# Kernel optimization log

Hardware: AMD Instinct MI355X
Metric: run time of the kernel (lower is better)

## Reference

```python
import jax, jax.numpy as jnp
import numpy as np

B, T_IN, F, H = 256, 168, 128, 512
T_OUT = 48


def setup_inputs() -> dict:
    key = jax.random.key(0)
    ks = jax.random.split(key, 8)
    s = 1.0 / np.sqrt(H)
    return {
        "x": jax.random.normal(ks[0], (B, T_IN, F), dtype=jnp.float32),
        "enc_Wih": jax.random.normal(ks[1], (4 * H, F), dtype=jnp.float32) * s,
        "enc_Whh": jax.random.normal(ks[2], (4 * H, H), dtype=jnp.float32) * s,
        "enc_b": jax.random.normal(ks[3], (4 * H,), dtype=jnp.float32) * s,
        "dec_Wih": jax.random.normal(ks[4], (4 * H, F), dtype=jnp.float32) * s,
        "dec_Whh": jax.random.normal(ks[5], (4 * H, H), dtype=jnp.float32) * s,
        "dec_b": jax.random.normal(ks[6], (4 * H,), dtype=jnp.float32) * s,
        "W_lin": jax.random.normal(ks[7], (F, H), dtype=jnp.float32) * s,
        "t_out": T_OUT,
    }


def _lstm_cell(h, c, xt, Wih, Whh, b):
    # torch gate order: i, f, g, o
    gates = xt @ Wih.T + h @ Whh.T + b  # [B, 4H]
    i, f, g, o = jnp.split(gates, 4, axis=-1)
    c_new = jax.nn.sigmoid(f) * c + jax.nn.sigmoid(i) * jnp.tanh(g)
    h_new = jax.nn.sigmoid(o) * jnp.tanh(c_new)
    return h_new, c_new


def reference(x, enc_Wih, enc_Whh, enc_b, dec_Wih, dec_Whh, dec_b, W_lin, t_out):
    bsz = x.shape[0]
    hidden = enc_Whh.shape[1]
    h0 = jnp.zeros((bsz, hidden), x.dtype)
    c0 = jnp.zeros((bsz, hidden), x.dtype)

    # ---- encoder: scan over T_in ----
    def enc_step(carry, xt):
        h, c = carry
        h, c = _lstm_cell(h, c, xt, enc_Wih, enc_Whh, enc_b)
        return (h, c), None

    (hn, cn), _ = jax.lax.scan(enc_step, (h0, c0), jnp.swapaxes(x, 0, 1))

    # ---- decoder: recursive feeding, scan over T_out ----
    dec_in0 = x[:, -1, :]  # [B, F]

    def dec_step(carry, _):
        h, c, inp = carry
        h, c = _lstm_cell(h, c, inp, dec_Wih, dec_Whh, dec_b)
        out = h @ W_lin.T  # [B, F]
        return (h, c, out), out

    _, outs = jax.lax.scan(dec_step, (hn, cn, dec_in0), None, length=t_out)
    return jnp.swapaxes(outs, 0, 1)  # [B, T_out, F]
```

## Files before the change

kernel.cpp:

```cpp
#include <hip/hip_runtime.h>
#include <hip/hip_bf16.h>

typedef __bf16 bf16_t;
typedef __bf16 bf16x8 __attribute__((ext_vector_type(8)));
typedef __bf16 bf16x4 __attribute__((ext_vector_type(4)));
typedef float  f32x4  __attribute__((ext_vector_type(4)));

#define HID 512
#define BATCH 256
#define TIN 168
#define TOUT 48
#define FEAT 128
#define NSTEPS (TIN + TOUT)
#define NGRP 8
#define NJT 32
#define GRPB 32

__device__ __forceinline__ float sigmoidf_(float x) {
    x = fminf(fmaxf(x, -30.f), 30.f);
    return 1.f / (1.f + __expf(-x));
}
__device__ __forceinline__ float tanhf_(float x) {
    x = fminf(fmaxf(x, -15.f), 15.f);
    float e = __expf(2.f * x);
    return (e - 1.f) / (e + 1.f);
}

__device__ __forceinline__ bf16x8 ld_h8(const bf16_t* p) {
    union { unsigned long long q[2]; bf16x8 v; } u;
    u.q[0] = __hip_atomic_load((const unsigned long long*)p,     __ATOMIC_RELAXED,
                               __HIP_MEMORY_SCOPE_SYSTEM);
    u.q[1] = __hip_atomic_load((const unsigned long long*)p + 1, __ATOMIC_RELAXED,
                               __HIP_MEMORY_SCOPE_SYSTEM);
    return u.v;
}
__device__ __forceinline__ void st_h(bf16_t* p, float v) {
    bf16_t b = (bf16_t)v;
    unsigned short u;
    __builtin_memcpy(&u, &b, 2);
    __hip_atomic_store((unsigned short*)p, u, __ATOMIC_RELAXED, __HIP_MEMORY_SCOPE_SYSTEM);
}

__global__ __launch_bounds__(256)
void cast_x_kernel(const float* __restrict__ x, bf16_t* __restrict__ Xbf) {
    int q = blockIdx.x * 256 + threadIdx.x;
    if (q >= BATCH * TIN * (FEAT / 4)) return;
    int f4  = q & 31;
    int rem = q >> 5;
    int t = rem % TIN;
    int b = rem / TIN;
    float4 v = *(const float4*)&x[((size_t)b * TIN + t) * FEAT + f4 * 4];
    bf16x4 o = { (bf16_t)v.x, (bf16_t)v.y, (bf16_t)v.z, (bf16_t)v.w };
    *(bf16x4*)&Xbf[((size_t)t * BATCH + b) * FEAT + f4 * 4] = o;
}

__global__ __launch_bounds__(256)
void cast_wcat_kernel(const float* __restrict__ Wih, const float* __restrict__ Whh,
                      bf16_t* __restrict__ Wcat) {
    int q = blockIdx.x * 256 + threadIdx.x;
    int k4 = q % 160;
    int r  = q / 160;
    if (r >= 2048) return;
    int k = k4 * 4;
    float4 v;
    if (k < FEAT) v = *(const float4*)&Wih[(size_t)r * FEAT + k];
    else          v = *(const float4*)&Whh[(size_t)r * HID + (k - FEAT)];
    bf16x4 o = { (bf16_t)v.x, (bf16_t)v.y, (bf16_t)v.z, (bf16_t)v.w };
    *(bf16x4*)&Wcat[(size_t)r * 640 + k] = o;
}

__global__ __launch_bounds__(256)
void cast_wlin_kernel(const float* __restrict__ W, bf16_t* __restrict__ Wb) {
    int q = blockIdx.x * 256 + threadIdx.x;
    if (q >= FEAT * HID / 4) return;
    float4 v = *(const float4*)&W[q * 4];
    bf16x4 o = { (bf16_t)v.x, (bf16_t)v.y, (bf16_t)v.z, (bf16_t)v.w };
    *(bf16x4*)&Wb[q * 4] = o;
}

__global__ __launch_bounds__(256)
void build_wcomb_kernel(const float* __restrict__ dWih, const float* __restrict__ dWhh,
                        const float* __restrict__ Wlin, bf16_t* __restrict__ Wcomb) {
    __shared__ float As[64][128];
    __shared__ float Bs[128][64];
    int r0 = blockIdx.x * 64, c0 = blockIdx.y * 64;
    int tid = threadIdx.x;
    for (int i = tid; i < 64 * 32; i += 256) {
        int rr = i >> 5, cc = (i & 31) << 2;
        *(float4*)&As[rr][cc] = *(const float4*)&dWih[(size_t)(r0 + rr) * 128 + cc];
    }
    for (int i = tid; i < 128 * 16; i += 256) {
        int kk = i >> 4, cc = (i & 15) << 2;
        *(float4*)&Bs[kk][cc] = *(const float4*)&Wlin[(size_t)kk * HID + c0 + cc];
    }
    __syncthreads();
    int tx = tid & 15, ty = tid >> 4;
    float acc[4][4] = {};
    for (int k = 0; k < 128; ++k) {
        float a[4], b[4];
        #pragma unroll
        for (int i = 0; i < 4; ++i) a[i] = As[ty * 4 + i][k];
        #pragma unroll
        for (int j = 0; j < 4; ++j) b[j] = Bs[k][tx * 4 + j];
        #pragma unroll
        for (int i = 0; i < 4; ++i)
            #pragma unroll
            for (int j = 0; j < 4; ++j) acc[i][j] += a[i] * b[j];
    }
    for (int i = 0; i < 4; ++i) {
        int r = r0 + ty * 4 + i;
        for (int j = 0; j < 4; ++j) {
            int cc = c0 + tx * 4 + j;
            Wcomb[(size_t)r * HID + cc] = (bf16_t)(acc[i][j] + dWhh[(size_t)r * HID + cc]);
        }
    }
}


__device__ __forceinline__ void cell_finish(
    f32x4 (&acc)[4], float (&cacc)[4], float (*Ex)[GRPB][18],
    int gp, int bh, int l4, int l15, int b0, int jcol,
    bf16_t* __restrict__ hnext)
{
    if (gp == 1) {
        #pragma unroll
        for (int q = 0; q < 4; ++q)
            #pragma unroll
            for (int r = 0; r < 4; ++r)
                Ex[q][bh * 16 + l4 * 4 + r][l15] = acc[q][r];
    }
    __syncthreads();
    if (gp == 0) {
        #pragma unroll
        for (int q = 0; q < 4; ++q)
            #pragma unroll
            for (int r = 0; r < 4; ++r)
                acc[q][r] += Ex[q][bh * 16 + l4 * 4 + r][l15];
        #pragma unroll
        for (int r = 0; r < 4; ++r) {
            float cn = sigmoidf_(acc[1][r]) * cacc[r] + sigmoidf_(acc[0][r]) * tanhf_(acc[2][r]);
            cacc[r] = cn;
            float hv = sigmoidf_(acc[3][r]) * tanhf_(cn);
            int row = b0 + l4 * 4 + r;
            st_h(hnext + (size_t)row * HID + jcol, hv);
        }
        asm volatile("s_waitcnt vmcnt(0)" ::: "memory");
    }
    __syncthreads();
}

__device__ __forceinline__ void group_wait(const unsigned int* flags, int g, int tid,
                                           unsigned int epoch) {
    if (tid < NJT) {
        while (__hip_atomic_load(&flags[g * NJT + tid], __ATOMIC_RELAXED,
                                 __HIP_MEMORY_SCOPE_SYSTEM) < epoch)
            __builtin_amdgcn_s_sleep(1);
    }
    __syncthreads();
}

__device__ __forceinline__ void group_arrive(unsigned int* flags, int g, int jt, int tid,
                                             unsigned int epoch) {
    if (tid == 0)
        __hip_atomic_store(&flags[g * NJT + jt], epoch, __ATOMIC_RELAXED,
                           __HIP_MEMORY_SCOPE_SYSTEM);
}

__global__ __launch_bounds__(256, 1)
void lstm_persist(const bf16_t* __restrict__ Xbf,
                  const bf16_t* __restrict__ Wenc, const float* __restrict__ enc_b,
                  const bf16_t* __restrict__ Wdec1, const bf16_t* __restrict__ Wcomb,
                  const float* __restrict__ dec_b,
                  bf16_t* __restrict__ hbufA, bf16_t* __restrict__ hbufB,
                  bf16_t* __restrict__ Hdec, unsigned int* __restrict__ flags)
{
    __shared__ float Ex[4][GRPB][18];
    const int bid = blockIdx.x;
    const int g   = bid & (NGRP - 1);
    const int jt  = bid >> 3;
    const int j0  = jt * 16;
    const int tid = threadIdx.x;
    const int wave = tid >> 6, lane = tid & 63;
    const int l15 = lane & 15, l4 = lane >> 4;
    const int bh = wave & 1, gp = wave >> 1;
    const int b0 = g * GRPB + bh * 16;
    const int arow = b0 + l15;
    const int jcol = j0 + l15;

    float biasE[4], biasD[4];
    #pragma unroll
    for (int q = 0; q < 4; ++q) {
        biasE[q] = enc_b[q * HID + jcol];
        biasD[q] = dec_b[q * HID + jcol];
    }
    float cacc[4] = {0.f, 0.f, 0.f, 0.f};

    bf16x8 Breg[40];
    const int kc0 = gp * 320;

    #pragma unroll
    for (int q = 0; q < 4; ++q)
        #pragma unroll
        for (int i = 0; i < 10; ++i)
            Breg[q * 10 + i] = *(const bf16x8*)(
                Wenc + (size_t)(q * HID + jcol) * 640 + kc0 + i * 32 + l4 * 8);
    #pragma unroll
    for (int n = 0; n < 40; ++n) asm volatile("" : "+v"(Breg[n]));

    for (int t = 0; t < TIN; ++t) {
        if (t > 0) group_wait(flags, g, tid, (unsigned)t);
        const bf16_t* hb = (t & 1) ? hbufB : hbufA;
        bf16_t* hn       = (t & 1) ? hbufA : hbufB;
        f32x4 acc[4];
        #pragma unroll
        for (int q = 0; q < 4; ++q) {
            float bv = (gp == 0) ? biasE[q] : 0.f;
            acc[q] = (f32x4){bv, bv, bv, bv};
        }
        const bf16_t* xb  = Xbf + ((size_t)t * BATCH + arow) * FEAT + l4 * 8;
        const bf16_t* hbp = hb + (size_t)arow * HID + l4 * 8;
        #pragma unroll
        for (int i = 0; i < 10; ++i) {
            int kc = kc0 + i * 32;
            bf16x8 a;
            if (kc < FEAT) a = *(const bf16x8*)(xb + kc);
            else           a = ld_h8(hbp + (kc - FEAT));
            #pragma unroll
            for (int q = 0; q < 4; ++q)
                acc[q] = __builtin_amdgcn_mfma_f32_16x16x32_bf16(a, Breg[q * 10 + i], acc[q], 0, 0, 0);
        }
        cell_finish(acc, cacc, Ex, gp, bh, l4, l15, b0, jcol, hn);
        group_arrive(flags, g, jt, tid, (unsigned)(t + 1));
    }

    #pragma unroll
    for (int q = 0; q < 4; ++q)
        #pragma unroll
        for (int i = 0; i < 10; ++i)
            Breg[q * 10 + i] = *(const bf16x8*)(
                Wdec1 + (size_t)(q * HID + jcol) * 640 + kc0 + i * 32 + l4 * 8);
    #pragma unroll
    for (int n = 0; n < 40; ++n) asm volatile("" : "+v"(Breg[n]));

    {
        const int t = TIN;
        group_wait(flags, g, tid, (unsigned)t);
        f32x4 acc[4];
        #pragma unroll
        for (int q = 0; q < 4; ++q) {
            float bv = (gp == 0) ? biasD[q] : 0.f;
            acc[q] = (f32x4){bv, bv, bv, bv};
        }
        const bf16_t* xb  = Xbf + ((size_t)(TIN - 1) * BATCH + arow) * FEAT + l4 * 8;
        const bf16_t* hbp = hbufA + (size_t)arow * HID + l4 * 8;
        #pragma unroll
        for (int i = 0; i < 10; ++i) {
            int kc = kc0 + i * 32;
            bf16x8 a;
            if (kc < FEAT) a = *(const bf16x8*)(xb + kc);
            else           a = ld_h8(hbp + (kc - FEAT));
            #pragma unroll
            for (int q = 0; q < 4; ++q)
                acc[q] = __builtin_amdgcn_mfma_f32_16x16x32_bf16(a, Breg[q * 10 + i], acc[q], 0, 0, 0);
        }
        cell_finish(acc, cacc, Ex, gp, bh, l4, l15, b0, jcol, Hdec);
        group_arrive(flags, g, jt, tid, (unsigned)(t + 1));
    }

    const int kd0 = gp * 256;
    #pragma unroll
    for (int q = 0; q < 4; ++q)
        #pragma unroll
        for (int i = 0; i < 8; ++i)
            Breg[q * 8 + i] = *(const bf16x8*)(
                Wcomb + (size_t)(q * HID + jcol) * HID + kd0 + i * 32 + l4 * 8);
    #pragma unroll
    for (int n = 0; n < 32; ++n) asm volatile("" : "+v"(Breg[n]));

    for (int t = TIN + 1; t < NSTEPS; ++t) {
        group_wait(flags, g, tid, (unsigned)t);
        const bf16_t* hprev = Hdec + (size_t)(t - 1 - TIN) * BATCH * HID
                                   + (size_t)arow * HID + l4 * 8;
        f32x4 acc[4];
        #pragma unroll
        for (int q = 0; q < 4; ++q) {
            float bv = (gp == 0) ? biasD[q] : 0.f;
            acc[q] = (f32x4){bv, bv, bv, bv};
        }
        #pragma unroll
        for (int i = 0; i < 8; ++i) {
            bf16x8 a = ld_h8(hprev + kd0 + i * 32);
            #pragma unroll
            for (int q = 0; q < 4; ++q)
                acc[q] = __builtin_amdgcn_mfma_f32_16x16x32_bf16(a, Breg[q * 8 + i], acc[q], 0, 0, 0);
        }
        cell_finish(acc, cacc, Ex, gp, bh, l4, l15, b0, jcol,
                    Hdec + (size_t)(t - TIN) * BATCH * HID);
        group_arrive(flags, g, jt, tid, (unsigned)(t + 1));
    }
}

__global__ __launch_bounds__(128)
void final_proj_kernel(const bf16_t* __restrict__ Hdec, const bf16_t* __restrict__ Wlin,
                       float* __restrict__ out) {
    int tid = threadIdx.x;
    int wv = tid >> 6, lane = tid & 63;
    int l15 = lane & 15, l4 = lane >> 4;
    int row0 = blockIdx.x * 32 + wv * 16;
    const bf16_t* arow = Hdec + (size_t)(row0 + l15) * HID;
    f32x4 acc[8];
    #pragma unroll
    for (int n = 0; n < 8; ++n) acc[n] = (f32x4){0.f, 0.f, 0.f, 0.f};
    #pragma unroll 4
    for (int kc = 0; kc < HID; kc += 32) {
        bf16x8 af = *(const bf16x8*)(arow + kc + l4 * 8);
        #pragma unroll
        for (int n = 0; n < 8; ++n) {
            bf16x8 bfr = *(const bf16x8*)(Wlin + (size_t)(n * 16 + l15) * HID + kc + l4 * 8);
            acc[n] = __builtin_amdgcn_mfma_f32_16x16x32_bf16(af, bfr, acc[n], 0, 0, 0);
        }
    }
    #pragma unroll
    for (int n = 0; n < 8; ++n) {
        int f = n * 16 + l15;
        #pragma unroll
        for (int r = 0; r < 4; ++r) {
            int row = row0 + l4 * 4 + r;
            int t = row >> 8;
            int b = row & 255;
            out[(size_t)b * (TOUT * FEAT) + (size_t)t * FEAT + f] = acc[n][r];
        }
    }
}

extern "C" void kernel_launch(void* const* d_in, const int* in_sizes, int n_in,
                              void* d_out, int out_size, void* d_ws, size_t ws_size,
                              hipStream_t stream) {
    const float* x       = (const float*)d_in[0];
    const float* enc_Wih = (const float*)d_in[1];
    const float* enc_Whh = (const float*)d_in[2];
    const float* enc_b   = (const float*)d_in[3];
    const float* dec_Wih = (const float*)d_in[4];
    const float* dec_Whh = (const float*)d_in[5];
    const float* dec_b   = (const float*)d_in[6];
    const float* W_lin   = (const float*)d_in[7];
    float* out = (float*)d_out;

    char* p = (char*)d_ws;
    auto alloc = [&](size_t bytes) -> void* {
        void* r = (void*)p;
        p += (bytes + 255) & ~(size_t)255;
        return r;
    };
    bf16_t* Xbf    = (bf16_t*)alloc((size_t)TIN * BATCH * FEAT * 2);
    bf16_t* Wenc   = (bf16_t*)alloc((size_t)2048 * 640 * 2);
    bf16_t* Wdec1  = (bf16_t*)alloc((size_t)2048 * 640 * 2);
    bf16_t* Wcomb  = (bf16_t*)alloc((size_t)2048 * HID * 2);
    bf16_t* Wlinb  = (bf16_t*)alloc((size_t)FEAT * HID * 2);
    bf16_t* hbufA  = (bf16_t*)alloc((size_t)BATCH * HID * 2);
    bf16_t* hbufB  = (bf16_t*)alloc((size_t)BATCH * HID * 2);
    bf16_t* Hdec   = (bf16_t*)alloc((size_t)TOUT * BATCH * HID * 2);
    unsigned int* flags = (unsigned int*)alloc((size_t)NGRP * NJT * 4);

    (void)hipMemsetAsync(hbufA, 0, (size_t)BATCH * HID * 2, stream);
    (void)hipMemsetAsync(flags, 0, (size_t)NGRP * NJT * 4, stream);

    cast_x_kernel<<<(BATCH * TIN * (FEAT / 4) + 255) / 256, 256, 0, stream>>>(x, Xbf);
    cast_wcat_kernel<<<(2048 * 160 + 255) / 256, 256, 0, stream>>>(enc_Wih, enc_Whh, Wenc);
    cast_wcat_kernel<<<(2048 * 160 + 255) / 256, 256, 0, stream>>>(dec_Wih, dec_Whh, Wdec1);
    cast_wlin_kernel<<<(FEAT * HID / 4 + 255) / 256, 256, 0, stream>>>(W_lin, Wlinb);
    build_wcomb_kernel<<<dim3(2048 / 64, HID / 64), 256, 0, stream>>>(dec_Wih, dec_Whh, W_lin, Wcomb);

    lstm_persist<<<NGRP * NJT, 256, 0, stream>>>(Xbf, Wenc, enc_b, Wdec1, Wcomb, dec_b,
                                                 hbufA, hbufB, Hdec, flags);

    final_proj_kernel<<<(TOUT * BATCH) / 32, 128, 0, stream>>>(Hdec, Wlinb, out);
}
```

Measured before the change: 1.054 ms.

## Use agent-scope atomics when a group's blocks share one XCC, and vectorize h stores

At kernel start each block records its XCC id, and each batch group checks whether all 32 of its blocks landed on the same XCC. If they did, the recurrence runs with agent-scope atomic loads, stores and flags, which can stay in the shared L2 instead of going to system-coherent memory. Otherwise it falls back to system scope. Separately, h outputs are staged through LDS and written as 16-byte vector stores instead of scattered 2-byte atomics. The fast path relies on the block-to-XCC dispatch placement, and the XCC check spin-waits across all blocks, which assumes every block is co-resident.

```diff
diff --git a/kernel.cpp b/kernel.cpp
--- a/kernel.cpp
+++ b/kernel.cpp
@@ -5,6 +5,7 @@
 typedef __bf16 bf16x8 __attribute__((ext_vector_type(8)));
 typedef __bf16 bf16x4 __attribute__((ext_vector_type(4)));
 typedef float  f32x4  __attribute__((ext_vector_type(4)));
+typedef unsigned long long u64;
 
 #define HID 512
 #define BATCH 256
@@ -26,19 +27,19 @@
     return (e - 1.f) / (e + 1.f);
 }
 
+template <int SCOPE>
 __device__ __forceinline__ bf16x8 ld_h8(const bf16_t* p) {
-    union { unsigned long long q[2]; bf16x8 v; } u;
-    u.q[0] = __hip_atomic_load((const unsigned long long*)p,     __ATOMIC_RELAXED,
-                               __HIP_MEMORY_SCOPE_SYSTEM);
-    u.q[1] = __hip_atomic_load((const unsigned long long*)p + 1, __ATOMIC_RELAXED,
-                               __HIP_MEMORY_SCOPE_SYSTEM);
+    union { u64 q[2]; bf16x8 v; } u;
+    u.q[0] = __hip_atomic_load((const u64*)p,     __ATOMIC_RELAXED, SCOPE);
+    u.q[1] = __hip_atomic_load((const u64*)p + 1, __ATOMIC_RELAXED, SCOPE);
     return u.v;
 }
-__device__ __forceinline__ void st_h(bf16_t* p, float v) {
-    bf16_t b = (bf16_t)v;
-    unsigned short u;
-    __builtin_memcpy(&u, &b, 2);
-    __hip_atomic_store((unsigned short*)p, u, __ATOMIC_RELAXED, __HIP_MEMORY_SCOPE_SYSTEM);
+template <int SCOPE>
+__device__ __forceinline__ void st_h16(bf16_t* p, bf16x8 v) {
+    union { bf16x8 v; u64 q[2]; } u;
+    u.v = v;
+    __hip_atomic_store((u64*)p,     u.q[0], __ATOMIC_RELAXED, SCOPE);
+    __hip_atomic_store((u64*)p + 1, u.q[1], __ATOMIC_RELAXED, SCOPE);
 }
 
 __global__ __launch_bounds__(256)
@@ -117,9 +118,10 @@
 }
 
 
+template <int SCOPE>
 __device__ __forceinline__ void cell_finish(
-    f32x4 (&acc)[4], float (&cacc)[4], float (*Ex)[GRPB][18],
-    int gp, int bh, int l4, int l15, int b0, int jcol,
+    f32x4 (&acc)[4], float (&cacc)[4], float (*Ex)[GRPB][18], bf16_t (*Hs)[16],
+    int gp, int bh, int l4, int l15, int lane, int gbase, int j0,
     bf16_t* __restrict__ hnext)
 {
     if (gp == 1) {
@@ -141,29 +143,166 @@
             float cn = sigmoidf_(acc[1][r]) * cacc[r] + sigmoidf_(acc[0][r]) * tanhf_(acc[2][r]);
             cacc[r] = cn;
             float hv = sigmoidf_(acc[3][r]) * tanhf_(cn);
-            int row = b0 + l4 * 4 + r;
-            st_h(hnext + (size_t)row * HID + jcol, hv);
+            Hs[bh * 16 + l4 * 4 + r][l15] = (bf16_t)hv;
+        }
+        if (lane < 32) {
+            int row  = bh * 16 + (lane >> 1);
+            int half = lane & 1;
+            bf16x8 v = *(const bf16x8*)&Hs[row][half * 8];
+            st_h16<SCOPE>(hnext + (size_t)(gbase + row) * HID + j0 + half * 8, v);
         }
         asm volatile("s_waitcnt vmcnt(0)" ::: "memory");
     }
     __syncthreads();
 }
 
+template <int SCOPE>
 __device__ __forceinline__ void group_wait(const unsigned int* flags, int g, int tid,
                                            unsigned int epoch) {
     if (tid < NJT) {
-        while (__hip_atomic_load(&flags[g * NJT + tid], __ATOMIC_RELAXED,
-                                 __HIP_MEMORY_SCOPE_SYSTEM) < epoch)
+        while (__hip_atomic_load(&flags[g * NJT + tid], __ATOMIC_RELAXED, SCOPE) < epoch)
             __builtin_amdgcn_s_sleep(1);
     }
     __syncthreads();
 }
 
+template <int SCOPE>
 __device__ __forceinline__ void group_arrive(unsigned int* flags, int g, int jt, int tid,
                                              unsigned int epoch) {
     if (tid == 0)
-        __hip_atomic_store(&flags[g * NJT + jt], epoch, __ATOMIC_RELAXED,
-                           __HIP_MEMORY_SCOPE_SYSTEM);
+        __hip_atomic_store(&flags[g * NJT + jt], epoch, __ATOMIC_RELAXED, SCOPE);
+}
+
+template <int SCOPE>
+__device__ void run_steps(const bf16_t* __restrict__ Xbf,
+                          const bf16_t* __restrict__ Wenc, const float* __restrict__ enc_b,
+                          const bf16_t* __restrict__ Wdec1, const bf16_t* __restrict__ Wcomb,
+                          const float* __restrict__ dec_b,
+                          bf16_t* __restrict__ hbufA, bf16_t* __restrict__ hbufB,
+                          bf16_t* __restrict__ Hdec, unsigned int* __restrict__ flags,
+                          float (*Ex)[GRPB][18], bf16_t (*Hs)[16],
+                          int g, int jt, int tid)
+{
+    const int j0  = jt * 16;
+    const int wave = tid >> 6, lane = tid & 63;
+    const int l15 = lane & 15, l4 = lane >> 4;
+    const int bh = wave & 1, gp = wave >> 1;
+    const int gbase = g * GRPB;
+    const int b0 = gbase + bh * 16;
+    const int arow = b0 + l15;
+    const int jcol = j0 + l15;
+
+    float biasE[4], biasD[4];
+    #pragma unroll
+    for (int q = 0; q < 4; ++q) {
+        biasE[q] = enc_b[q * HID + jcol];
+        biasD[q] = dec_b[q * HID + jcol];
+    }
+    float cacc[4] = {0.f, 0.f, 0.f, 0.f};
+
+    bf16x8 Breg[40];
+    const int kc0 = gp * 320;
+
+    #pragma unroll
+    for (int q = 0; q < 4; ++q)
+        #pragma unroll
+        for (int i = 0; i < 10; ++i)
+            Breg[q * 10 + i] = *(const bf16x8*)(
+                Wenc + (size_t)(q * HID + jcol) * 640 + kc0 + i * 32 + l4 * 8);
+    #pragma unroll
+    for (int n = 0; n < 40; ++n) asm volatile("" : "+v"(Breg[n]));
+
+    for (int t = 0; t < TIN; ++t) {
+        if (t > 0) group_wait<SCOPE>(flags, g, tid, (unsigned)t);
+        const bf16_t* hb = (t & 1) ? hbufB : hbufA;
+        bf16_t* hn       = (t & 1) ? hbufA : hbufB;
+        f32x4 acc[4];
+        #pragma unroll
+        for (int q = 0; q < 4; ++q) {
+            float bv = (gp == 0) ? biasE[q] : 0.f;
+            acc[q] = (f32x4){bv, bv, bv, bv};
+        }
+        const bf16_t* xb  = Xbf + ((size_t)t * BATCH + arow) * FEAT + l4 * 8;
+        const bf16_t* hbp = hb + (size_t)arow * HID + l4 * 8;
+        #pragma unroll
+        for (int i = 0; i < 10; ++i) {
+            int kc = kc0 + i * 32;
+            bf16x8 a;
+            if (kc < FEAT) a = *(const bf16x8*)(xb + kc);
+            else           a = ld_h8<SCOPE>(hbp + (kc - FEAT));
+            #pragma unroll
+            for (int q = 0; q < 4; ++q)
+                acc[q] = __builtin_amdgcn_mfma_f32_16x16x32_bf16(a, Breg[q * 10 + i], acc[q], 0, 0, 0);
+        }
+        cell_finish<SCOPE>(acc, cacc, Ex, Hs, gp, bh, l4, l15, lane, gbase, j0, hn);
+        group_arrive<SCOPE>(flags, g, jt, tid, (unsigned)(t + 1));
+    }
+
+    #pragma unroll
+    for (int q = 0; q < 4; ++q)
+        #pragma unroll
+        for (int i = 0; i < 10; ++i)
+            Breg[q * 10 + i] = *(const bf16x8*)(
+                Wdec1 + (size_t)(q * HID + jcol) * 640 + kc0 + i * 32 + l4 * 8);
+    #pragma unroll
+    for (int n = 0; n < 40; ++n) asm volatile("" : "+v"(Breg[n]));
+
+    {
+        const int t = TIN;
+        group_wait<SCOPE>(flags, g, tid, (unsigned)t);
+        f32x4 acc[4];
+        #pragma unroll
+        for (int q = 0; q < 4; ++q) {
+            float bv = (gp == 0) ? biasD[q] : 0.f;
+            acc[q] = (f32x4){bv, bv, bv, bv};
+        }
+        const bf16_t* xb  = Xbf + ((size_t)(TIN - 1) * BATCH + arow) * FEAT + l4 * 8;
+        const bf16_t* hbp = hbufA + (size_t)arow * HID + l4 * 8;
+        #pragma unroll
+        for (int i = 0; i < 10; ++i) {
+            int kc = kc0 + i * 32;
+            bf16x8 a;
+            if (kc < FEAT) a = *(const bf16x8*)(xb + kc);
+            else           a = ld_h8<SCOPE>(hbp + (kc - FEAT));
+            #pragma unroll
+            for (int q = 0; q < 4; ++q)
+                acc[q] = __builtin_amdgcn_mfma_f32_16x16x32_bf16(a, Breg[q * 10 + i], acc[q], 0, 0, 0);
+        }
+        cell_finish<SCOPE>(acc, cacc, Ex, Hs, gp, bh, l4, l15, lane, gbase, j0, Hdec);
+        group_arrive<SCOPE>(flags, g, jt, tid, (unsigned)(t + 1));
+    }
+
+    const int kd0 = gp * 256;
+    #pragma unroll
+    for (int q = 0; q < 4; ++q)
+        #pragma unroll
+        for (int i = 0; i < 8; ++i)
+            Breg[q * 8 + i] = *(const bf16x8*)(
+                Wcomb + (size_t)(q * HID + jcol) * HID + kd0 + i * 32 + l4 * 8);
+    #pragma unroll
+    for (int n = 0; n < 32; ++n) asm volatile("" : "+v"(Breg[n]));
+
+    for (int t = TIN + 1; t < NSTEPS; ++t) {
+        group_wait<SCOPE>(flags, g, tid, (unsigned)t);
+        const bf16_t* hprev = Hdec + (size_t)(t - 1 - TIN) * BATCH * HID
+                                   + (size_t)arow * HID + l4 * 8;
+        f32x4 acc[4];
+        #pragma unroll
+        for (int q = 0; q < 4; ++q) {
+            float bv = (gp == 0) ? biasD[q] : 0.f;
+            acc[q] = (f32x4){bv, bv, bv, bv};
+        }
+        #pragma unroll
+        for (int i = 0; i < 8; ++i) {
+            bf16x8 a = ld_h8<SCOPE>(hprev + kd0 + i * 32);
+            #pragma unroll
+            for (int q = 0; q < 4; ++q)
+                acc[q] = __builtin_amdgcn_mfma_f32_16x16x32_bf16(a, Breg[q * 8 + i], acc[q], 0, 0, 0);
+        }
+        cell_finish<SCOPE>(acc, cacc, Ex, Hs, gp, bh, l4, l15, lane, gbase, j0,
+                           Hdec + (size_t)(t - TIN) * BATCH * HID);
+        group_arrive<SCOPE>(flags, g, jt, tid, (unsigned)(t + 1));
+    }
 }
 
 __global__ __launch_bounds__(256, 1)
@@ -172,132 +311,45 @@
                   const bf16_t* __restrict__ Wdec1, const bf16_t* __restrict__ Wcomb,
                   const float* __restrict__ dec_b,
                   bf16_t* __restrict__ hbufA, bf16_t* __restrict__ hbufB,
-                  bf16_t* __restrict__ Hdec, unsigned int* __restrict__ flags)
+                  bf16_t* __restrict__ Hdec, unsigned int* __restrict__ flags,
+                  unsigned int* __restrict__ xccbuf)
 {
-    __shared__ float Ex[4][GRPB][18];
+    __shared__ float  Ex[4][GRPB][18];
+    __shared__ bf16_t Hs[GRPB][16];
+    __shared__ int    fastflag;
     const int bid = blockIdx.x;
     const int g   = bid & (NGRP - 1);
     const int jt  = bid >> 3;
-    const int j0  = jt * 16;
     const int tid = threadIdx.x;
-    const int wave = tid >> 6, lane = tid & 63;
-    const int l15 = lane & 15, l4 = lane >> 4;
-    const int bh = wave & 1, gp = wave >> 1;
-    const int b0 = g * GRPB + bh * 16;
-    const int arow = b0 + l15;
-    const int jcol = j0 + l15;
-
-    float biasE[4], biasD[4];
-    #pragma unroll
-    for (int q = 0; q < 4; ++q) {
-        biasE[q] = enc_b[q * HID + jcol];
-        biasD[q] = dec_b[q * HID + jcol];
-    }
-    float cacc[4] = {0.f, 0.f, 0.f, 0.f};
-
-    bf16x8 Breg[40];
-    const int kc0 = gp * 320;
-
-    #pragma unroll
-    for (int q = 0; q < 4; ++q)
-        #pragma unroll
-        for (int i = 0; i < 10; ++i)
-            Breg[q * 10 + i] = *(const bf16x8*)(
-                Wenc + (size_t)(q * HID + jcol) * 640 + kc0 + i * 32 + l4 * 8);
-    #pragma unroll
-    for (int n = 0; n < 40; ++n) asm volatile("" : "+v"(Breg[n]));
-
-    for (int t = 0; t < TIN; ++t) {
-        if (t > 0) group_wait(flags, g, tid, (unsigned)t);
-        const bf16_t* hb = (t & 1) ? hbufB : hbufA;
-        bf16_t* hn       = (t & 1) ? hbufA : hbufB;
-        f32x4 acc[4];
-        #pragma unroll
-        for (int q = 0; q < 4; ++q) {
-            float bv = (gp == 0) ? biasE[q] : 0.f;
-            acc[q] = (f32x4){bv, bv, bv, bv};
-        }
-        const bf16_t* xb  = Xbf + ((size_t)t * BATCH + arow) * FEAT + l4 * 8;
-        const bf16_t* hbp = hb + (size_t)arow * HID + l4 * 8;
-        #pragma unroll
-        for (int i = 0; i < 10; ++i) {
-            int kc = kc0 + i * 32;
-            bf16x8 a;
-            if (kc < FEAT) a = *(const bf16x8*)(xb + kc);
-            else           a = ld_h8(hbp + (kc - FEAT));
-            #pragma unroll
-            for (int q = 0; q < 4; ++q)
-                acc[q] = __builtin_amdgcn_mfma_f32_16x16x32_bf16(a, Breg[q * 10 + i], acc[q], 0, 0, 0);
-        }
-        cell_finish(acc, cacc, Ex, gp, bh, l4, l15, b0, jcol, hn);
-        group_arrive(flags, g, jt, tid, (unsigned)(t + 1));
-    }
-
-    #pragma unroll
-    for (int q = 0; q < 4; ++q)
-        #pragma unroll
-        for (int i = 0; i < 10; ++i)
-            Breg[q * 10 + i] = *(const bf16x8*)(
-                Wdec1 + (size_t)(q * HID + jcol) * 640 + kc0 + i * 32 + l4 * 8);
-    #pragma unroll
-    for (int n = 0; n < 40; ++n) asm volatile("" : "+v"(Breg[n]));
-
-    {
-        const int t = TIN;
-        group_wait(flags, g, tid, (unsigned)t);
-        f32x4 acc[4];
-        #pragma unroll
-        for (int q = 0; q < 4; ++q) {
-            float bv = (gp == 0) ? biasD[q] : 0.f;
-            acc[q] = (f32x4){bv, bv, bv, bv};
-        }
-        const bf16_t* xb  = Xbf + ((size_t)(TIN - 1) * BATCH + arow) * FEAT + l4 * 8;
-        const bf16_t* hbp = hbufA + (size_t)arow * HID + l4 * 8;
-        #pragma unroll
-        for (int i = 0; i < 10; ++i) {
-            int kc = kc0 + i * 32;
-            bf16x8 a;
-            if (kc < FEAT) a = *(const bf16x8*)(xb + kc);
-            else           a = ld_h8(hbp + (kc - FEAT));
-            #pragma unroll
-            for (int q = 0; q < 4; ++q)
-                acc[q] = __builtin_amdgcn_mfma_f32_16x16x32_bf16(a, Breg[q * 10 + i], acc[q], 0, 0, 0);
-        }
-        cell_finish(acc, cacc, Ex, gp, bh, l4, l15, b0, jcol, Hdec);
-        group_arrive(flags, g, jt, tid, (unsigned)(t + 1));
-    }
-
-    const int kd0 = gp * 256;
-    #pragma unroll
-    for (int q = 0; q < 4; ++q)
-        #pragma unroll
-        for (int i = 0; i < 8; ++i)
-            Breg[q * 8 + i] = *(const bf16x8*)(
-                Wcomb + (size_t)(q * HID + jcol) * HID + kd0 + i * 32 + l4 * 8);
-    #pragma unroll
-    for (int n = 0; n < 32; ++n) asm volatile("" : "+v"(Breg[n]));
-
-    for (int t = TIN + 1; t < NSTEPS; ++t) {
-        group_wait(flags, g, tid, (unsigned)t);
-        const bf16_t* hprev = Hdec + (size_t)(t - 1 - TIN) * BATCH * HID
-                                   + (size_t)arow * HID + l4 * 8;
-        f32x4 acc[4];
-        #pragma unroll
-        for (int q = 0; q < 4; ++q) {
-            float bv = (gp == 0) ? biasD[q] : 0.f;
-            acc[q] = (f32x4){bv, bv, bv, bv};
-        }
-        #pragma unroll
-        for (int i = 0; i < 8; ++i) {
-            bf16x8 a = ld_h8(hprev + kd0 + i * 32);
-            #pragma unroll
-            for (int q = 0; q < 4; ++q)
-                acc[q] = __builtin_amdgcn_mfma_f32_16x16x32_bf16(a, Breg[q * 8 + i], acc[q], 0, 0, 0);
-        }
-        cell_finish(acc, cacc, Ex, gp, bh, l4, l15, b0, jcol,
-                    Hdec + (size_t)(t - TIN) * BATCH * HID);
-        group_arrive(flags, g, jt, tid, (unsigned)(t + 1));
-    }
+    const int lane = tid & 63;
+
+    unsigned int xcc;
+    asm volatile("s_getreg_b32 %0, hwreg(HW_REG_XCC_ID)" : "=s"(xcc));
+    if (tid == 0)
+        __hip_atomic_store(&xccbuf[bid], xcc + 1u, __ATOMIC_RELAXED,
+                           __HIP_MEMORY_SCOPE_SYSTEM);
+    if (tid < 64) {
+        unsigned int v = 0;
+        if (lane < NJT) {
+            do {
+                v = __hip_atomic_load(&xccbuf[g + NGRP * lane], __ATOMIC_RELAXED,
+                                      __HIP_MEMORY_SCOPE_SYSTEM);
+                if (v == 0) __builtin_amdgcn_s_sleep(1);
+            } while (v == 0);
+        }
+        bool ok = (lane >= NJT) || (v == xcc + 1u);
+        unsigned long long m = __ballot(ok);
+        if (lane == 0) fastflag = (m == ~0ull) ? 1 : 0;
+    }
+    __syncthreads();
+    const bool fast = (fastflag != 0);
+
+    if (fast)
+        run_steps<__HIP_MEMORY_SCOPE_AGENT>(Xbf, Wenc, enc_b, Wdec1, Wcomb, dec_b,
+                                            hbufA, hbufB, Hdec, flags, Ex, Hs, g, jt, tid);
+    else
+        run_steps<__HIP_MEMORY_SCOPE_SYSTEM>(Xbf, Wenc, enc_b, Wdec1, Wcomb, dec_b,
+                                             hbufA, hbufB, Hdec, flags, Ex, Hs, g, jt, tid);
 }
 
 __global__ __launch_bounds__(128)
@@ -360,10 +412,12 @@
     bf16_t* hbufA  = (bf16_t*)alloc((size_t)BATCH * HID * 2);
     bf16_t* hbufB  = (bf16_t*)alloc((size_t)BATCH * HID * 2);
     bf16_t* Hdec   = (bf16_t*)alloc((size_t)TOUT * BATCH * HID * 2);
-    unsigned int* flags = (unsigned int*)alloc((size_t)NGRP * NJT * 4);
+    unsigned int* flags  = (unsigned int*)alloc((size_t)NGRP * NJT * 4);
+    unsigned int* xccbuf = (unsigned int*)alloc((size_t)NGRP * NJT * 4);
 
     (void)hipMemsetAsync(hbufA, 0, (size_t)BATCH * HID * 2, stream);
     (void)hipMemsetAsync(flags, 0, (size_t)NGRP * NJT * 4, stream);
+    (void)hipMemsetAsync(xccbuf, 0, (size_t)NGRP * NJT * 4, stream);
 
     cast_x_kernel<<<(BATCH * TIN * (FEAT / 4) + 255) / 256, 256, 0, stream>>>(x, Xbf);
     cast_wcat_kernel<<<(2048 * 160 + 255) / 256, 256, 0, stream>>>(enc_Wih, enc_Whh, Wenc);
@@ -372,7 +426,7 @@
     build_wcomb_kernel<<<dim3(2048 / 64, HID / 64), 256, 0, stream>>>(dec_Wih, dec_Whh, W_lin, Wcomb);
 
     lstm_persist<<<NGRP * NJT, 256, 0, stream>>>(Xbf, Wenc, enc_b, Wdec1, Wcomb, dec_b,
-                                                 hbufA, hbufB, Hdec, flags);
+                                                 hbufA, hbufB, Hdec, flags, xccbuf);
 
     final_proj_kernel<<<(TOUT * BATCH) / 32, 128, 0, stream>>>(Hdec, Wlinb, out);
 }
```

New measurement: 1.177 ms. +11.7%, slower.

## Replace block barriers with per-wave flag polling and double-buffered exchange

Applied to the files above, without the earlier changes.

Each wave now polls the group's readiness flags itself with a wave-wide vote, instead of a few threads polling and then a block barrier. Each half-batch wave publishes its own flag, so there are 64 flags per group and only one __syncthreads per step. The LDS exchange buffer is double-buffered by step parity so the trailing barrier can be dropped. The x-input loads are issued before the wait, and all hidden-state loads are batched before the MFMAs to overlap memory latency. The risks are heavier flag-polling traffic and relying on parity buffering being enough for correctness.

```diff
diff --git a/kernel.cpp b/kernel.cpp
--- a/kernel.cpp
+++ b/kernel.cpp
@@ -5,6 +5,7 @@
 typedef __bf16 bf16x8 __attribute__((ext_vector_type(8)));
 typedef __bf16 bf16x4 __attribute__((ext_vector_type(4)));
 typedef float  f32x4  __attribute__((ext_vector_type(4)));
+typedef unsigned long long u64;
 
 #define HID 512
 #define BATCH 256
@@ -27,10 +28,10 @@
 }
 
 __device__ __forceinline__ bf16x8 ld_h8(const bf16_t* p) {
-    union { unsigned long long q[2]; bf16x8 v; } u;
-    u.q[0] = __hip_atomic_load((const unsigned long long*)p,     __ATOMIC_RELAXED,
+    union { u64 q[2]; bf16x8 v; } u;
+    u.q[0] = __hip_atomic_load((const u64*)p,     __ATOMIC_RELAXED,
                                __HIP_MEMORY_SCOPE_SYSTEM);
-    u.q[1] = __hip_atomic_load((const unsigned long long*)p + 1, __ATOMIC_RELAXED,
+    u.q[1] = __hip_atomic_load((const u64*)p + 1, __ATOMIC_RELAXED,
                                __HIP_MEMORY_SCOPE_SYSTEM);
     return u.v;
 }
@@ -117,53 +118,39 @@
 }
 
 
-__device__ __forceinline__ void cell_finish(
-    f32x4 (&acc)[4], float (&cacc)[4], float (*Ex)[GRPB][18],
-    int gp, int bh, int l4, int l15, int b0, int jcol,
-    bf16_t* __restrict__ hnext)
+__device__ __forceinline__ void group_wait(const unsigned int* flags, int g, int lane,
+                                           unsigned int epoch) {
+    const unsigned int* fp = &flags[g * 64 + lane];
+    for (;;) {
+        unsigned int v = __hip_atomic_load(fp, __ATOMIC_RELAXED,
+                                           __HIP_MEMORY_SCOPE_SYSTEM);
+        if (__all((int)(v >= epoch))) break;
+        __builtin_amdgcn_s_sleep(1);
+    }
+}
+
+__device__ __forceinline__ void cell_store(
+    f32x4 (&acc)[4], float (&cacc)[4], const float (*Exp)[GRPB][17],
+    unsigned int* flags, int g, int jt, int bh, int lane, int l4, int l15,
+    int b0, int jcol, unsigned int epoch_next, bf16_t* __restrict__ hnext)
 {
-    if (gp == 1) {
-        #pragma unroll
-        for (int q = 0; q < 4; ++q)
-            #pragma unroll
-            for (int r = 0; r < 4; ++r)
-                Ex[q][bh * 16 + l4 * 4 + r][l15] = acc[q][r];
-    }
-    __syncthreads();
-    if (gp == 0) {
-        #pragma unroll
-        for (int q = 0; q < 4; ++q)
-            #pragma unroll
-            for (int r = 0; r < 4; ++r)
-                acc[q][r] += Ex[q][bh * 16 + l4 * 4 + r][l15];
-        #pragma unroll
-        for (int r = 0; r < 4; ++r) {
-            float cn = sigmoidf_(acc[1][r]) * cacc[r] + sigmoidf_(acc[0][r]) * tanhf_(acc[2][r]);
-            cacc[r] = cn;
-            float hv = sigmoidf_(acc[3][r]) * tanhf_(cn);
-            int row = b0 + l4 * 4 + r;
-            st_h(hnext + (size_t)row * HID + jcol, hv);
-        }
-        asm volatile("s_waitcnt vmcnt(0)" ::: "memory");
-    }
-    __syncthreads();
-}
-
-__device__ __forceinline__ void group_wait(const unsigned int* flags, int g, int tid,
-                                           unsigned int epoch) {
-    if (tid < NJT) {
-        while (__hip_atomic_load(&flags[g * NJT + tid], __ATOMIC_RELAXED,
-                                 __HIP_MEMORY_SCOPE_SYSTEM) < epoch)
-            __builtin_amdgcn_s_sleep(1);
-    }
-    __syncthreads();
-}
-
-__device__ __forceinline__ void group_arrive(unsigned int* flags, int g, int jt, int tid,
-                                             unsigned int epoch) {
-    if (tid == 0)
-        __hip_atomic_store(&flags[g * NJT + jt], epoch, __ATOMIC_RELAXED,
-                           __HIP_MEMORY_SCOPE_SYSTEM);
+    #pragma unroll
+    for (int q = 0; q < 4; ++q)
+        #pragma unroll
+        for (int r = 0; r < 4; ++r)
+            acc[q][r] += Exp[q][bh * 16 + l4 * 4 + r][l15];
+    #pragma unroll
+    for (int r = 0; r < 4; ++r) {
+        float cn = sigmoidf_(acc[1][r]) * cacc[r] + sigmoidf_(acc[0][r]) * tanhf_(acc[2][r]);
+        cacc[r] = cn;
+        float hv = sigmoidf_(acc[3][r]) * tanhf_(cn);
+        int row = b0 + l4 * 4 + r;
+        st_h(hnext + (size_t)row * HID + jcol, hv);
+    }
+    asm volatile("s_waitcnt vmcnt(0)" ::: "memory");
+    if (lane == 0)
+        __hip_atomic_store(&flags[g * 64 + jt * 2 + bh], epoch_next,
+                           __ATOMIC_RELAXED, __HIP_MEMORY_SCOPE_SYSTEM);
 }
 
 __global__ __launch_bounds__(256, 1)
@@ -174,7 +161,7 @@
                   bf16_t* __restrict__ hbufA, bf16_t* __restrict__ hbufB,
                   bf16_t* __restrict__ Hdec, unsigned int* __restrict__ flags)
 {
-    __shared__ float Ex[4][GRPB][18];
+    __shared__ float Ex[2][4][GRPB][17];
     const int bid = blockIdx.x;
     const int g   = bid & (NGRP - 1);
     const int jt  = bid >> 3;
@@ -208,29 +195,46 @@
     for (int n = 0; n < 40; ++n) asm volatile("" : "+v"(Breg[n]));
 
     for (int t = 0; t < TIN; ++t) {
-        if (t > 0) group_wait(flags, g, tid, (unsigned)t);
+        const int par = t & 1;
         const bf16_t* hb = (t & 1) ? hbufB : hbufA;
         bf16_t* hn       = (t & 1) ? hbufA : hbufB;
+        bf16x8 a[10];
+        const bf16_t* xb = Xbf + ((size_t)t * BATCH + arow) * FEAT + l4 * 8;
+        if (gp == 0) {
+            #pragma unroll
+            for (int i = 0; i < 4; ++i) a[i] = *(const bf16x8*)(xb + i * 32);
+        }
+        if (t > 0) group_wait(flags, g, lane, (unsigned)t);
+        const bf16_t* hbp = hb + (size_t)arow * HID + l4 * 8;
+        if (gp == 0) {
+            #pragma unroll
+            for (int i = 4; i < 10; ++i) a[i] = ld_h8(hbp + (i * 32 - FEAT));
+        } else {
+            #pragma unroll
+            for (int i = 0; i < 10; ++i) a[i] = ld_h8(hbp + (320 - FEAT) + i * 32);
+        }
         f32x4 acc[4];
         #pragma unroll
         for (int q = 0; q < 4; ++q) {
             float bv = (gp == 0) ? biasE[q] : 0.f;
             acc[q] = (f32x4){bv, bv, bv, bv};
         }
-        const bf16_t* xb  = Xbf + ((size_t)t * BATCH + arow) * FEAT + l4 * 8;
-        const bf16_t* hbp = hb + (size_t)arow * HID + l4 * 8;
-        #pragma unroll
-        for (int i = 0; i < 10; ++i) {
-            int kc = kc0 + i * 32;
-            bf16x8 a;
-            if (kc < FEAT) a = *(const bf16x8*)(xb + kc);
-            else           a = ld_h8(hbp + (kc - FEAT));
-            #pragma unroll
-            for (int q = 0; q < 4; ++q)
-                acc[q] = __builtin_amdgcn_mfma_f32_16x16x32_bf16(a, Breg[q * 10 + i], acc[q], 0, 0, 0);
-        }
-        cell_finish(acc, cacc, Ex, gp, bh, l4, l15, b0, jcol, hn);
-        group_arrive(flags, g, jt, tid, (unsigned)(t + 1));
+        #pragma unroll
+        for (int i = 0; i < 10; ++i)
+            #pragma unroll
+            for (int q = 0; q < 4; ++q)
+                acc[q] = __builtin_amdgcn_mfma_f32_16x16x32_bf16(a[i], Breg[q * 10 + i], acc[q], 0, 0, 0);
+        if (gp == 1) {
+            #pragma unroll
+            for (int q = 0; q < 4; ++q)
+                #pragma unroll
+                for (int r = 0; r < 4; ++r)
+                    Ex[par][q][bh * 16 + l4 * 4 + r][l15] = acc[q][r];
+        }
+        __syncthreads();
+        if (gp == 0)
+            cell_store(acc, cacc, Ex[par], flags, g, jt, bh, lane, l4, l15,
+                       b0, jcol, (unsigned)(t + 1), hn);
     }
 
     #pragma unroll
@@ -244,27 +248,44 @@
 
     {
         const int t = TIN;
-        group_wait(flags, g, tid, (unsigned)t);
+        const int par = t & 1;
+        bf16x8 a[10];
+        const bf16_t* xb = Xbf + ((size_t)(TIN - 1) * BATCH + arow) * FEAT + l4 * 8;
+        if (gp == 0) {
+            #pragma unroll
+            for (int i = 0; i < 4; ++i) a[i] = *(const bf16x8*)(xb + i * 32);
+        }
+        group_wait(flags, g, lane, (unsigned)t);
+        const bf16_t* hbp = hbufA + (size_t)arow * HID + l4 * 8;
+        if (gp == 0) {
+            #pragma unroll
+            for (int i = 4; i < 10; ++i) a[i] = ld_h8(hbp + (i * 32 - FEAT));
+        } else {
+            #pragma unroll
+            for (int i = 0; i < 10; ++i) a[i] = ld_h8(hbp + (320 - FEAT) + i * 32);
+        }
         f32x4 acc[4];
         #pragma unroll
         for (int q = 0; q < 4; ++q) {
             float bv = (gp == 0) ? biasD[q] : 0.f;
             acc[q] = (f32x4){bv, bv, bv, bv};
         }
-        const bf16_t* xb  = Xbf + ((size_t)(TIN - 1) * BATCH + arow) * FEAT + l4 * 8;
-        const bf16_t* hbp = hbufA + (size_t)arow * HID + l4 * 8;
-        #pragma unroll
-        for (int i = 0; i < 10; ++i) {
-            int kc = kc0 + i * 32;
-            bf16x8 a;
-            if (kc < FEAT) a = *(const bf16x8*)(xb + kc);
-            else           a = ld_h8(hbp + (kc - FEAT));
-            #pragma unroll
-            for (int q = 0; q < 4; ++q)
-                acc[q] = __builtin_amdgcn_mfma_f32_16x16x32_bf16(a, Breg[q * 10 + i], acc[q], 0, 0, 0);
-        }
-        cell_finish(acc, cacc, Ex, gp, bh, l4, l15, b0, jcol, Hdec);
-        group_arrive(flags, g, jt, tid, (unsigned)(t + 1));
+        #pragma unroll
+        for (int i = 0; i < 10; ++i)
+            #pragma unroll
+            for (int q = 0; q < 4; ++q)
+                acc[q] = __builtin_amdgcn_mfma_f32_16x16x32_bf16(a[i], Breg[q * 10 + i], acc[q], 0, 0, 0);
+        if (gp == 1) {
+            #pragma unroll
+            for (int q = 0; q < 4; ++q)
+                #pragma unroll
+                for (int r = 0; r < 4; ++r)
+                    Ex[par][q][bh * 16 + l4 * 4 + r][l15] = acc[q][r];
+        }
+        __syncthreads();
+        if (gp == 0)
+            cell_store(acc, cacc, Ex[par], flags, g, jt, bh, lane, l4, l15,
+                       b0, jcol, (unsigned)(t + 1), Hdec);
     }
 
     const int kd0 = gp * 256;
@@ -278,9 +299,14 @@
     for (int n = 0; n < 32; ++n) asm volatile("" : "+v"(Breg[n]));
 
     for (int t = TIN + 1; t < NSTEPS; ++t) {
-        group_wait(flags, g, tid, (unsigned)t);
+        const int par = t & 1;
+        group_wait(flags, g, lane, (unsigned)t);
         const bf16_t* hprev = Hdec + (size_t)(t - 1 - TIN) * BATCH * HID
                                    + (size_t)arow * HID + l4 * 8;
+        bf16x8 a[8];
+        #pragma unroll
+        for (int i = 0; i < 8; ++i)
+            a[i] = ld_h8(hprev + kd0 + i * 32);
         f32x4 acc[4];
         #pragma unroll
         for (int q = 0; q < 4; ++q) {
@@ -288,15 +314,22 @@
             acc[q] = (f32x4){bv, bv, bv, bv};
         }
         #pragma unroll
-        for (int i = 0; i < 8; ++i) {
-            bf16x8 a = ld_h8(hprev + kd0 + i * 32);
-            #pragma unroll
-            for (int q = 0; q < 4; ++q)
-                acc[q] = __builtin_amdgcn_mfma_f32_16x16x32_bf16(a, Breg[q * 8 + i], acc[q], 0, 0, 0);
-        }
-        cell_finish(acc, cacc, Ex, gp, bh, l4, l15, b0, jcol,
-                    Hdec + (size_t)(t - TIN) * BATCH * HID);
-        group_arrive(flags, g, jt, tid, (unsigned)(t + 1));
+        for (int i = 0; i < 8; ++i)
+            #pragma unroll
+            for (int q = 0; q < 4; ++q)
+                acc[q] = __builtin_amdgcn_mfma_f32_16x16x32_bf16(a[i], Breg[q * 8 + i], acc[q], 0, 0, 0);
+        if (gp == 1) {
+            #pragma unroll
+            for (int q = 0; q < 4; ++q)
+                #pragma unroll
+                for (int r = 0; r < 4; ++r)
+                    Ex[par][q][bh * 16 + l4 * 4 + r][l15] = acc[q][r];
+        }
+        __syncthreads();
+        if (gp == 0)
+            cell_store(acc, cacc, Ex[par], flags, g, jt, bh, lane, l4, l15,
+                       b0, jcol, (unsigned)(t + 1),
+                       Hdec + (size_t)(t - TIN) * BATCH * HID);
     }
 }
 
@@ -360,10 +393,10 @@
     bf16_t* hbufA  = (bf16_t*)alloc((size_t)BATCH * HID * 2);
     bf16_t* hbufB  = (bf16_t*)alloc((size_t)BATCH * HID * 2);
     bf16_t* Hdec   = (bf16_t*)alloc((size_t)TOUT * BATCH * HID * 2);
-    unsigned int* flags = (unsigned int*)alloc((size_t)NGRP * NJT * 4);
+    unsigned int* flags = (unsigned int*)alloc((size_t)NGRP * 64 * 4);
 
     (void)hipMemsetAsync(hbufA, 0, (size_t)BATCH * HID * 2, stream);
-    (void)hipMemsetAsync(flags, 0, (size_t)NGRP * NJT * 4, stream);
+    (void)hipMemsetAsync(flags, 0, (size_t)NGRP * 64 * 4, stream);
 
     cast_x_kernel<<<(BATCH * TIN * (FEAT / 4) + 255) / 256, 256, 0, stream>>>(x, Xbf);
     cast_wcat_kernel<<<(2048 * 160 + 255) / 256, 256, 0, stream>>>(enc_Wih, enc_Whh, Wenc);
```

New measurement: 2.162 ms. 105% more time.

## Swap MFMA operands for packed 4-wide h stores and batch loads ahead of MFMAs

Applied to the files above, without the earlier changes.

Swaps the A/B operands of the MFMA so each lane's accumulator holds four consecutive hidden columns of one batch row. The new hidden state can then be written with a single 64-bit atomic store instead of four 16-bit stores, and the cross-wave exchange in LDS becomes one float4 per lane. All A-fragment loads are issued before the MFMA chain so global-load latency overlaps, and biases are loaded as float4. The cost is more live registers for the staged A fragments, on top of the 40 persistent weight registers.

```diff
diff --git a/kernel.cpp b/kernel.cpp
--- a/kernel.cpp
+++ b/kernel.cpp
@@ -5,6 +5,8 @@
 typedef __bf16 bf16x8 __attribute__((ext_vector_type(8)));
 typedef __bf16 bf16x4 __attribute__((ext_vector_type(4)));
 typedef float  f32x4  __attribute__((ext_vector_type(4)));
+typedef unsigned int u32;
+typedef unsigned long long u64;
 
 #define HID 512
 #define BATCH 256
@@ -27,18 +29,20 @@
 }
 
 __device__ __forceinline__ bf16x8 ld_h8(const bf16_t* p) {
-    union { unsigned long long q[2]; bf16x8 v; } u;
-    u.q[0] = __hip_atomic_load((const unsigned long long*)p,     __ATOMIC_RELAXED,
+    union { u64 q[2]; bf16x8 v; } u;
+    u.q[0] = __hip_atomic_load((const u64*)p,     __ATOMIC_RELAXED,
                                __HIP_MEMORY_SCOPE_SYSTEM);
-    u.q[1] = __hip_atomic_load((const unsigned long long*)p + 1, __ATOMIC_RELAXED,
+    u.q[1] = __hip_atomic_load((const u64*)p + 1, __ATOMIC_RELAXED,
                                __HIP_MEMORY_SCOPE_SYSTEM);
     return u.v;
 }
-__device__ __forceinline__ void st_h(bf16_t* p, float v) {
-    bf16_t b = (bf16_t)v;
-    unsigned short u;
-    __builtin_memcpy(&u, &b, 2);
-    __hip_atomic_store((unsigned short*)p, u, __ATOMIC_RELAXED, __HIP_MEMORY_SCOPE_SYSTEM);
+__device__ __forceinline__ void st_h4(bf16_t* p, float v0, float v1, float v2, float v3) {
+    bf16_t b0 = (bf16_t)v0, b1 = (bf16_t)v1, b2 = (bf16_t)v2, b3 = (bf16_t)v3;
+    unsigned short s0, s1, s2, s3;
+    __builtin_memcpy(&s0, &b0, 2); __builtin_memcpy(&s1, &b1, 2);
+    __builtin_memcpy(&s2, &b2, 2); __builtin_memcpy(&s3, &b3, 2);
+    u64 w = (u64)s0 | ((u64)s1 << 16) | ((u64)s2 << 32) | ((u64)s3 << 48);
+    __hip_atomic_store((u64*)p, w, __ATOMIC_RELAXED, __HIP_MEMORY_SCOPE_SYSTEM);
 }
 
 __global__ __launch_bounds__(256)
@@ -117,39 +121,7 @@
 }
 
 
-__device__ __forceinline__ void cell_finish(
-    f32x4 (&acc)[4], float (&cacc)[4], float (*Ex)[GRPB][18],
-    int gp, int bh, int l4, int l15, int b0, int jcol,
-    bf16_t* __restrict__ hnext)
-{
-    if (gp == 1) {
-        #pragma unroll
-        for (int q = 0; q < 4; ++q)
-            #pragma unroll
-            for (int r = 0; r < 4; ++r)
-                Ex[q][bh * 16 + l4 * 4 + r][l15] = acc[q][r];
-    }
-    __syncthreads();
-    if (gp == 0) {
-        #pragma unroll
-        for (int q = 0; q < 4; ++q)
-            #pragma unroll
-            for (int r = 0; r < 4; ++r)
-                acc[q][r] += Ex[q][bh * 16 + l4 * 4 + r][l15];
-        #pragma unroll
-        for (int r = 0; r < 4; ++r) {
-            float cn = sigmoidf_(acc[1][r]) * cacc[r] + sigmoidf_(acc[0][r]) * tanhf_(acc[2][r]);
-            cacc[r] = cn;
-            float hv = sigmoidf_(acc[3][r]) * tanhf_(cn);
-            int row = b0 + l4 * 4 + r;
-            st_h(hnext + (size_t)row * HID + jcol, hv);
-        }
-        asm volatile("s_waitcnt vmcnt(0)" ::: "memory");
-    }
-    __syncthreads();
-}
-
-__device__ __forceinline__ void group_wait(const unsigned int* flags, int g, int tid,
+__device__ __forceinline__ void group_wait(const u32* flags, int g, int tid,
                                            unsigned int epoch) {
     if (tid < NJT) {
         while (__hip_atomic_load(&flags[g * NJT + tid], __ATOMIC_RELAXED,
@@ -159,11 +131,39 @@
     __syncthreads();
 }
 
-__device__ __forceinline__ void group_arrive(unsigned int* flags, int g, int jt, int tid,
+__device__ __forceinline__ void group_arrive(u32* flags, int g, int jt, int tid,
                                              unsigned int epoch) {
     if (tid == 0)
         __hip_atomic_store(&flags[g * NJT + jt], epoch, __ATOMIC_RELAXED,
                            __HIP_MEMORY_SCOPE_SYSTEM);
+}
+
+__device__ __forceinline__ void cell_finish(
+    f32x4 (&acc)[4], float (&cacc)[4], f32x4 (*Ex)[2][64],
+    int gp, int bh, int lane, int l15, int l4, int brow, int jq0,
+    bf16_t* __restrict__ hnext)
+{
+    if (gp == 1) {
+        #pragma unroll
+        for (int q = 0; q < 4; ++q)
+            Ex[q][bh][lane] = acc[q];
+    }
+    __syncthreads();
+    if (gp == 0) {
+        #pragma unroll
+        for (int q = 0; q < 4; ++q)
+            acc[q] += Ex[q][bh][lane];
+        float hv[4];
+        #pragma unroll
+        for (int r = 0; r < 4; ++r) {
+            float cn = sigmoidf_(acc[1][r]) * cacc[r] + sigmoidf_(acc[0][r]) * tanhf_(acc[2][r]);
+            cacc[r] = cn;
+            hv[r] = sigmoidf_(acc[3][r]) * tanhf_(cn);
+        }
+        st_h4(hnext + (size_t)brow * HID + jq0, hv[0], hv[1], hv[2], hv[3]);
+        asm volatile("s_waitcnt vmcnt(0)" ::: "memory");
+    }
+    __syncthreads();
 }
 
 __global__ __launch_bounds__(256, 1)
@@ -172,9 +172,9 @@
                   const bf16_t* __restrict__ Wdec1, const bf16_t* __restrict__ Wcomb,
                   const float* __restrict__ dec_b,
                   bf16_t* __restrict__ hbufA, bf16_t* __restrict__ hbufB,
-                  bf16_t* __restrict__ Hdec, unsigned int* __restrict__ flags)
+                  bf16_t* __restrict__ Hdec, u32* __restrict__ flags)
 {
-    __shared__ float Ex[4][GRPB][18];
+    __shared__ f32x4 Ex[4][2][64];
     const int bid = blockIdx.x;
     const int g   = bid & (NGRP - 1);
     const int jt  = bid >> 3;
@@ -186,12 +186,13 @@
     const int b0 = g * GRPB + bh * 16;
     const int arow = b0 + l15;
     const int jcol = j0 + l15;
-
-    float biasE[4], biasD[4];
+    const int jq0  = j0 + l4 * 4;
+
+    f32x4 biasE4[4], biasD4[4];
     #pragma unroll
     for (int q = 0; q < 4; ++q) {
-        biasE[q] = enc_b[q * HID + jcol];
-        biasD[q] = dec_b[q * HID + jcol];
+        biasE4[q] = *(const f32x4*)&enc_b[q * HID + jq0];
+        biasD4[q] = *(const f32x4*)&dec_b[q * HID + jq0];
     }
     float cacc[4] = {0.f, 0.f, 0.f, 0.f};
 
@@ -211,25 +212,28 @@
         if (t > 0) group_wait(flags, g, tid, (unsigned)t);
         const bf16_t* hb = (t & 1) ? hbufB : hbufA;
         bf16_t* hn       = (t & 1) ? hbufA : hbufB;
-        f32x4 acc[4];
-        #pragma unroll
-        for (int q = 0; q < 4; ++q) {
-            float bv = (gp == 0) ? biasE[q] : 0.f;
-            acc[q] = (f32x4){bv, bv, bv, bv};
-        }
         const bf16_t* xb  = Xbf + ((size_t)t * BATCH + arow) * FEAT + l4 * 8;
         const bf16_t* hbp = hb + (size_t)arow * HID + l4 * 8;
-        #pragma unroll
-        for (int i = 0; i < 10; ++i) {
-            int kc = kc0 + i * 32;
-            bf16x8 a;
-            if (kc < FEAT) a = *(const bf16x8*)(xb + kc);
-            else           a = ld_h8(hbp + (kc - FEAT));
+        bf16x8 a[10];
+        if (gp == 0) {
+            #pragma unroll
+            for (int i = 0; i < 4; ++i)  a[i] = *(const bf16x8*)(xb + i * 32);
+            #pragma unroll
+            for (int i = 4; i < 10; ++i) a[i] = ld_h8(hbp + (i * 32 - FEAT));
+        } else {
+            #pragma unroll
+            for (int i = 0; i < 10; ++i) a[i] = ld_h8(hbp + (320 - FEAT) + i * 32);
+        }
+        f32x4 acc[4];
+        #pragma unroll
+        for (int q = 0; q < 4; ++q)
+            acc[q] = (gp == 0) ? biasE4[q] : (f32x4){0.f, 0.f, 0.f, 0.f};
+        #pragma unroll
+        for (int i = 0; i < 10; ++i)
             #pragma unroll
             for (int q = 0; q < 4; ++q)
-                acc[q] = __builtin_amdgcn_mfma_f32_16x16x32_bf16(a, Breg[q * 10 + i], acc[q], 0, 0, 0);
-        }
-        cell_finish(acc, cacc, Ex, gp, bh, l4, l15, b0, jcol, hn);
+                acc[q] = __builtin_amdgcn_mfma_f32_16x16x32_bf16(Breg[q * 10 + i], a[i], acc[q], 0, 0, 0);
+        cell_finish(acc, cacc, Ex, gp, bh, lane, l15, l4, arow, jq0, hn);
         group_arrive(flags, g, jt, tid, (unsigned)(t + 1));
     }
 
@@ -245,25 +249,28 @@
     {
         const int t = TIN;
         group_wait(flags, g, tid, (unsigned)t);
-        f32x4 acc[4];
-        #pragma unroll
-        for (int q = 0; q < 4; ++q) {
-            float bv = (gp == 0) ? biasD[q] : 0.f;
-            acc[q] = (f32x4){bv, bv, bv, bv};
-        }
         const bf16_t* xb  = Xbf + ((size_t)(TIN - 1) * BATCH + arow) * FEAT + l4 * 8;
         const bf16_t* hbp = hbufA + (size_t)arow * HID + l4 * 8;
-        #pragma unroll
-        for (int i = 0; i < 10; ++i) {
-            int kc = kc0 + i * 32;
-            bf16x8 a;
-            if (kc < FEAT) a = *(const bf16x8*)(xb + kc);
-            else           a = ld_h8(hbp + (kc - FEAT));
+        bf16x8 a[10];
+        if (gp == 0) {
+            #pragma unroll
+            for (int i = 0; i < 4; ++i)  a[i] = *(const bf16x8*)(xb + i * 32);
+            #pragma unroll
+            for (int i = 4; i < 10; ++i) a[i] = ld_h8(hbp + (i * 32 - FEAT));
+        } else {
+            #pragma unroll
+            for (int i = 0; i < 10; ++i) a[i] = ld_h8(hbp + (320 - FEAT) + i * 32);
+        }
+        f32x4 acc[4];
+        #pragma unroll
+        for (int q = 0; q < 4; ++q)
+            acc[q] = (gp == 0) ? biasD4[q] : (f32x4){0.f, 0.f, 0.f, 0.f};
+        #pragma unroll
+        for (int i = 0; i < 10; ++i)
             #pragma unroll
             for (int q = 0; q < 4; ++q)
-                acc[q] = __builtin_amdgcn_mfma_f32_16x16x32_bf16(a, Breg[q * 10 + i], acc[q], 0, 0, 0);
-        }
-        cell_finish(acc, cacc, Ex, gp, bh, l4, l15, b0, jcol, Hdec);
+                acc[q] = __builtin_amdgcn_mfma_f32_16x16x32_bf16(Breg[q * 10 + i], a[i], acc[q], 0, 0, 0);
+        cell_finish(acc, cacc, Ex, gp, bh, lane, l15, l4, arow, jq0, Hdec);
         group_arrive(flags, g, jt, tid, (unsigned)(t + 1));
     }
 
@@ -281,20 +288,20 @@
         group_wait(flags, g, tid, (unsigned)t);
         const bf16_t* hprev = Hdec + (size_t)(t - 1 - TIN) * BATCH * HID
                                    + (size_t)arow * HID + l4 * 8;
+        bf16x8 a[8];
+        #pragma unroll
+        for (int i = 0; i < 8; ++i)
+            a[i] = ld_h8(hprev + kd0 + i * 32);
         f32x4 acc[4];
         #pragma unroll
-        for (int q = 0; q < 4; ++q) {
-            float bv = (gp == 0) ? biasD[q] : 0.f;
-            acc[q] = (f32x4){bv, bv, bv, bv};
-        }
-        #pragma unroll
-        for (int i = 0; i < 8; ++i) {
-            bf16x8 a = ld_h8(hprev + kd0 + i * 32);
+        for (int q = 0; q < 4; ++q)
+            acc[q] = (gp == 0) ? biasD4[q] : (f32x4){0.f, 0.f, 0.f, 0.f};
+        #pragma unroll
+        for (int i = 0; i < 8; ++i)
             #pragma unroll
             for (int q = 0; q < 4; ++q)
-                acc[q] = __builtin_amdgcn_mfma_f32_16x16x32_bf16(a, Breg[q * 8 + i], acc[q], 0, 0, 0);
-        }
-        cell_finish(acc, cacc, Ex, gp, bh, l4, l15, b0, jcol,
+                acc[q] = __builtin_amdgcn_mfma_f32_16x16x32_bf16(Breg[q * 8 + i], a[i], acc[q], 0, 0, 0);
+        cell_finish(acc, cacc, Ex, gp, bh, lane, l15, l4, arow, jq0,
                     Hdec + (size_t)(t - TIN) * BATCH * HID);
         group_arrive(flags, g, jt, tid, (unsigned)(t + 1));
     }
@@ -360,7 +367,7 @@
     bf16_t* hbufA  = (bf16_t*)alloc((size_t)BATCH * HID * 2);
     bf16_t* hbufB  = (bf16_t*)alloc((size_t)BATCH * HID * 2);
     bf16_t* Hdec   = (bf16_t*)alloc((size_t)TOUT * BATCH * HID * 2);
-    unsigned int* flags = (unsigned int*)alloc((size_t)NGRP * NJT * 4);
+    u32* flags     = (u32*)alloc((size_t)NGRP * NJT * 4);
 
     (void)hipMemsetAsync(hbufA, 0, (size_t)BATCH * HID * 2, stream);
     (void)hipMemsetAsync(flags, 0, (size_t)NGRP * NJT * 4, stream);
```

Result: faster. 1.004 ms, median of 2 (-4.7%).
